# Optimization experiments

Hardware: AMD Instinct MI355X
Metric: run time of the kernel (lower is better)

The kernel has to match this reference:

```python
import jax, jax.numpy as jnp
import numpy as np

N0, N1, N2 = 100000, 25000, 6250
F = 128
OUT = 5


def _mean_agg(feat_src, src, dst, n_dst):
    # DGL copy_u + mean: segment mean over destination nodes (0 for isolated dst)
    s = jax.ops.segment_sum(feat_src[src], dst, num_segments=n_dst)
    cnt = jax.ops.segment_sum(jnp.ones_like(dst, dtype=feat_src.dtype), dst, num_segments=n_dst)
    return s / jnp.maximum(cnt, 1.0)[:, None]


def _graph_conv(feat, src, dst, W, b, n):
    # DGL GraphConv, norm='both': D_src^-1/2 gather-sum D_dst^-1/2, then linear
    dt = feat.dtype
    out_deg = jax.ops.segment_sum(jnp.ones_like(src, dtype=dt), src, num_segments=n)
    in_deg = jax.ops.segment_sum(jnp.ones_like(dst, dtype=dt), dst, num_segments=n)
    ns = jnp.where(out_deg > 0, out_deg ** -0.5, 0.0)
    nd = jnp.where(in_deg > 0, in_deg ** -0.5, 0.0)
    agg = jax.ops.segment_sum((feat * ns[:, None])[src], dst, num_segments=n)
    return (agg * nd[:, None]) @ W + b


def setup_inputs() -> dict:
    key = jax.random.key(0)
    keys = jax.random.split(key, 64)
    _c = iter(range(64))
    def nrm(shape, s=0.05):
        return jax.random.normal(keys[next(_c)], shape, dtype=jnp.float32) * s
    def ri(n, hi):
        return jax.random.randint(keys[next(_c)], (n,), 0, hi)
    inp = {
        'X': nrm((N0, 32), 1.0),
        'g0_src': ri(1600000, N0), 'g0_dst': ri(1600000, N0),
        'g1_src': ri(400000, N1), 'g1_dst': ri(400000, N1),
        'g2_src': ri(100000, N2), 'g2_dst': ri(100000, N2),
        'inc0_src': ri(100000, N0), 'inc0_dst': ri(100000, N1),
        'inc1_src': ri(25000, N1), 'inc1_dst': ri(25000, N2),
        'dec0_src': ri(100000, N2), 'dec0_dst': ri(100000, N1),
        'dec1_src': ri(400000, N1), 'dec1_dst': ri(400000, N0),
        'W_emb': nrm((32, F)), 'b_emb': jnp.zeros((F,), jnp.float32),
        'W_gcn0': nrm((F, F)), 'b_gcn0': jnp.zeros((F,), jnp.float32),
        'W_gcn1': nrm((F, F)), 'b_gcn1': jnp.zeros((F,), jnp.float32),
        'W_gcn2': nrm((F, F)), 'b_gcn2': jnp.zeros((F,), jnp.float32),
        'W_enc0': nrm((F, F)), 'b_enc0': jnp.zeros((F,), jnp.float32),
        'W_enc1': nrm((F, F)), 'b_enc1': jnp.zeros((F,), jnp.float32),
        'W_dec0': nrm((F, F)), 'b_dec0': jnp.zeros((F,), jnp.float32),
        'W_dec1': nrm((F, F)), 'b_dec1': jnp.zeros((F,), jnp.float32),
        'W_head0': nrm((2 * F, OUT)), 'b_head0': jnp.zeros((OUT,), jnp.float32),
        'W_head1': nrm((2 * F, OUT)), 'b_head1': jnp.zeros((OUT,), jnp.float32),
        'W_head2': nrm((2 * F, OUT)), 'b_head2': jnp.zeros((OUT,), jnp.float32),
    }
    return inp


def reference(X, g0_src, g0_dst, g1_src, g1_dst, g2_src, g2_dst,
              inc0_src, inc0_dst, inc1_src, inc1_dst,
              dec0_src, dec0_dst, dec1_src, dec1_dst,
              W_emb, b_emb, W_gcn0, b_gcn0, W_gcn1, b_gcn1, W_gcn2, b_gcn2,
              W_enc0, b_enc0, W_enc1, b_enc1, W_dec0, b_dec0, W_dec1, b_dec1,
              W_head0, b_head0, W_head1, b_head1, W_head2, b_head2):
    # embedding at finest scale
    h0 = X @ W_emb + b_emb                                   # [N0, F]
    # encode + pool fine -> coarse (copy_u/mean)
    h1 = _mean_agg(h0 @ W_enc0 + b_enc0, inc0_src, inc0_dst, N1)   # [N1, F]
    h2 = _mean_agg(h1 @ W_enc1 + b_enc1, inc1_src, inc1_dst, N2)   # [N2, F]
    # intra-scale GraphConv
    g0 = _graph_conv(h0, g0_src, g0_dst, W_gcn0, b_gcn0, N0)
    g1 = _graph_conv(h1, g1_src, g1_dst, W_gcn1, b_gcn1, N1)
    g2 = _graph_conv(h2, g2_src, g2_dst, W_gcn2, b_gcn2, N2)
    # decode coarse -> fine
    d2 = g2
    d1 = _mean_agg(d2 @ W_dec0 + b_dec0, dec0_src, dec0_dst, N1)   # [N1, F]
    d0 = _mean_agg(d1 @ W_dec1 + b_dec1, dec1_src, dec1_dst, N0)   # [N0, F]
    # per-scale heads with softmax
    o0 = jax.nn.softmax(jnp.concatenate([g0, d0], -1) @ W_head0 + b_head0, axis=-1)
    o1 = jax.nn.softmax(jnp.concatenate([g1, d1], -1) @ W_head1 + b_head1, axis=-1)
    o2 = jax.nn.softmax(jnp.concatenate([g2, d2], -1) @ W_head2 + b_head2, axis=-1)
    return jnp.concatenate([o0, o1, o2], axis=0)             # [N0+N1+N2, OUT]
```

## Files before the change

kernel.cpp:

```cpp
#include <hip/hip_runtime.h>

#define F 128
static const int N0 = 100000, N1 = 25000, N2 = 6250;

typedef unsigned short u16;
typedef unsigned int   u32;
typedef __attribute__((ext_vector_type(8))) short bf16x8;
typedef __attribute__((ext_vector_type(4))) float f32x4;

__device__ __forceinline__ float bf2f(u16 u) {
    union { u32 i; float f; } v; v.i = ((u32)u) << 16; return v.f;
}
__device__ __forceinline__ u16 f2bf(float f) {
    u32 u = __float_as_uint(f);
    u += 0x7fff + ((u >> 16) & 1);
    return (u16)(u >> 16);
}

struct Seg7 {
    const int* src[7];
    const int* dst[7];
    int end[7];
    int cbase[7];
    int obase[7];
};

#define EPT 4
#define CEPT 4
#define SM32  (64*(32+8)*2 + 128*(32+8)*2 + 128*4)
#define SM128 (64*(128+8)*2 + 128*(128+8)*2 + 128*4)


template <int K, bool AF32, bool MASK>
__device__ __forceinline__ void dev_mm(char* smem, const void* __restrict__ Ap,
                                       const float* __restrict__ W,
                                       const float* __restrict__ bias,
                                       u16* __restrict__ out,
                                       const int* __restrict__ rowptr,
                                       int M, int blk) {
    const int AST = K + 8;
    const int WST = K + 8;
    u16* Al = (u16*)smem;
    u16* Wt = (u16*)(smem + 64 * AST * 2);
    float* bl = (float*)(smem + 64 * AST * 2 + 128 * WST * 2);
    int tid = threadIdx.x;
    int m0 = blk * 64;

    for (int i = tid; i < K * 128; i += 256) {
        int k = i >> 7, n = i & 127;
        Wt[n * WST + k] = f2bf(W[i]);
    }
    for (int i = tid; i < 64 * K; i += 256) {
        int r = i / K, c = i % K;
        int gr = m0 + r;
        u16 v = 0;
        if (gr < M) {
            if (AF32) v = f2bf(((const float*)Ap)[(size_t)gr * K + c]);
            else      v = ((const u16*)Ap)[(size_t)gr * K + c];
        }
        Al[r * AST + c] = v;
    }
    if (tid < 128) bl[tid] = bias[tid];
    __syncthreads();

    int w = tid >> 6;
    int lane = tid & 63;
    int m16 = lane & 15;
    int quad = lane >> 4;

    f32x4 acc[8];
#pragma unroll
    for (int t = 0; t < 8; t++)
#pragma unroll
        for (int r = 0; r < 4; r++) acc[t][r] = 0.f;

    for (int k0 = 0; k0 < K; k0 += 32) {
        bf16x8 af = *(const bf16x8*)&Al[(w * 16 + m16) * AST + k0 + quad * 8];
#pragma unroll
        for (int t = 0; t < 8; t++) {
            bf16x8 bf = *(const bf16x8*)&Wt[(t * 16 + m16) * WST + k0 + quad * 8];
            acc[t] = __builtin_amdgcn_mfma_f32_16x16x32_bf16(af, bf, acc[t], 0, 0, 0);
        }
    }

#pragma unroll
    for (int t = 0; t < 8; t++) {
#pragma unroll
        for (int r = 0; r < 4; r++) {
            int gr = m0 + w * 16 + quad * 4 + r;
            if (gr >= M) continue;
            int gc = t * 16 + m16;
            bool zrow = false;
            if (MASK) zrow = (rowptr[gr + 1] == rowptr[gr]);
            float v = acc[t][r] + bl[gc];
            out[(size_t)gr * F + gc] = zrow ? (u16)0 : f2bf(v);
        }
    }
}

template <int MODE>
__device__ __forceinline__ void dev_gather(const u16* __restrict__ feat,
                                           const int* __restrict__ rowptr,
                                           const int* __restrict__ col,
                                           const float* __restrict__ odr,
                                           u16* __restrict__ out, int M, int blk) {
    int wv = (blk * 256 + (int)threadIdx.x) >> 6;
    if (wv >= M) return;
    int lane = threadIdx.x & 63;
    int fo = lane << 1;
    int beg = rowptr[wv], end = rowptr[wv + 1];
    float a0 = 0.f, a1 = 0.f;
    int j = beg;
    for (; j + 8 <= end; j += 8) {
        int cc[8];
#pragma unroll
        for (int t = 0; t < 8; t++) cc[t] = col[j + t];
        float ss[8];
#pragma unroll
        for (int t = 0; t < 8; t++) ss[t] = (MODE == 1) ? odr[cc[t]] : 1.f;
        ushort2 uu[8];
#pragma unroll
        for (int t = 0; t < 8; t++) uu[t] = *(const ushort2*)&feat[(size_t)cc[t] * F + fo];
#pragma unroll
        for (int t = 0; t < 8; t++) { a0 += bf2f(uu[t].x) * ss[t]; a1 += bf2f(uu[t].y) * ss[t]; }
    }
    for (; j < end; j++) {
        int c = col[j];
        float s = (MODE == 1) ? odr[c] : 1.f;
        ushort2 u = *(const ushort2*)&feat[(size_t)c * F + fo];
        a0 += bf2f(u.x) * s; a1 += bf2f(u.y) * s;
    }
    int deg = end - beg;
    float fs = (MODE == 0) ? (deg > 0 ? 1.f / (float)deg : 0.f)
                           : (deg > 0 ? rsqrtf((float)deg) : 0.f);
    ushort2 o; o.x = f2bf(a0 * fs); o.y = f2bf(a1 * fs);
    *(ushort2*)&out[(size_t)wv * F + fo] = o;
}

template <bool GD>
__device__ __forceinline__ void dev_head(char* smem, const u16* __restrict__ g,
                                         const u16* __restrict__ d,
                                         const int* __restrict__ rowptr,
                                         const int* __restrict__ col,
                                         const float* __restrict__ Wh,
                                         const float* __restrict__ bh,
                                         float* __restrict__ out, int M, int blk) {
    float* Wl = (float*)smem;
    float* bl = (float*)(smem + 1280 * 4);
    int tid = threadIdx.x;
    for (int i = tid; i < 1280; i += 256) Wl[i] = Wh[i];
    if (tid < 5) bl[tid] = bh[tid];
    __syncthreads();

    int lane = tid & 63;
    int wv = tid >> 6;
    int r0 = blk * 32 + wv * 8;
    int k0 = lane << 1;
    for (int i = 0; i < 8; i++) {
        int row = r0 + i;
        if (row < M) {
            float d0v, d1v;
            if (GD) {
                int beg = rowptr[row], end = rowptr[row + 1];
                d0v = 0.f; d1v = 0.f;
                int j = beg;
                for (; j + 4 <= end; j += 4) {
                    int c0 = col[j], c1 = col[j + 1], c2 = col[j + 2], c3 = col[j + 3];
                    ushort2 u0 = *(const ushort2*)&d[(size_t)c0 * F + k0];
                    ushort2 u1 = *(const ushort2*)&d[(size_t)c1 * F + k0];
                    ushort2 u2 = *(const ushort2*)&d[(size_t)c2 * F + k0];
                    ushort2 u3 = *(const ushort2*)&d[(size_t)c3 * F + k0];
                    d0v += bf2f(u0.x) + bf2f(u1.x) + bf2f(u2.x) + bf2f(u3.x);
                    d1v += bf2f(u0.y) + bf2f(u1.y) + bf2f(u2.y) + bf2f(u3.y);
                }
                for (; j < end; j++) {
                    int c = col[j];
                    ushort2 u = *(const ushort2*)&d[(size_t)c * F + k0];
                    d0v += bf2f(u.x); d1v += bf2f(u.y);
                }
                int deg = end - beg;
                float fs = deg > 0 ? 1.f / (float)deg : 0.f;
                d0v *= fs; d1v *= fs;
            } else {
                ushort2 du = *(const ushort2*)&d[(size_t)row * F + k0];
                d0v = bf2f(du.x); d1v = bf2f(du.y);
            }
            ushort2 gu = *(const ushort2*)&g[(size_t)row * F + k0];
            float g0v = bf2f(gu.x), g1v = bf2f(gu.y);
            float p[5];
#pragma unroll
            for (int o = 0; o < 5; o++) {
                p[o] = g0v * Wl[k0 * 5 + o] + g1v * Wl[(k0 + 1) * 5 + o] +
                       d0v * Wl[(k0 + 128) * 5 + o] + d1v * Wl[(k0 + 129) * 5 + o];
            }
#pragma unroll
            for (int o = 0; o < 5; o++) {
                float v = p[o];
                v += __shfl_xor(v, 32, 64);
                v += __shfl_xor(v, 16, 64);
                v += __shfl_xor(v, 8, 64);
                v += __shfl_xor(v, 4, 64);
                v += __shfl_xor(v, 2, 64);
                v += __shfl_xor(v, 1, 64);
                p[o] = v + bl[o];
            }
            if (lane == 0) {
                float m = p[0];
#pragma unroll
                for (int o = 1; o < 5; o++) m = fmaxf(m, p[o]);
                float e[5], s = 0.f;
#pragma unroll
                for (int o = 0; o < 5; o++) { e[o] = expf(p[o] - m); s += e[o]; }
                float inv = 1.f / s;
#pragma unroll
                for (int o = 0; o < 5; o++) out[(size_t)row * 5 + o] = e[o] * inv;
            }
        }
    }
}


__global__ __launch_bounds__(256) void k_count_emb(Seg7 S, int* __restrict__ cnt,
                                                   int* __restrict__ od,
                                                   u16* __restrict__ occ, int ETOT,
                                                   const float* __restrict__ X,
                                                   const float* __restrict__ Wemb,
                                                   const float* __restrict__ bemb,
                                                   u16* __restrict__ h0, int nbMM) {
    __shared__ char smem[SM32];
    if ((int)blockIdx.x < nbMM) {
        dev_mm<32, true, false>(smem, X, Wemb, bemb, h0, nullptr, N0, blockIdx.x);
        return;
    }
    int base = ((int)blockIdx.x - nbMM) * (256 * CEPT) + threadIdx.x;
    int ee[CEPT], grow[CEPT], gs[CEPT];
#pragma unroll
    for (int t = 0; t < CEPT; t++) {
        int e = base + t * 256;
        ee[t] = e;
        grow[t] = -1; gs[t] = -1;
        if (e < ETOT) {
            int s = 0;
            while (e >= S.end[s]) s++;
            int le = e - ((s == 0) ? 0 : S.end[s - 1]);
            grow[t] = S.cbase[s] + S.dst[s][le];
            int ob = S.obase[s];
            if (ob >= 0) gs[t] = ob + S.src[s][le];
        }
    }
    u32 r[CEPT];
#pragma unroll
    for (int t = 0; t < CEPT; t++)
        if (grow[t] >= 0) r[t] = atomicAdd((u32*)&cnt[grow[t]], 1u);
#pragma unroll
    for (int t = 0; t < CEPT; t++)
        if (grow[t] >= 0) occ[ee[t]] = (u16)r[t];
#pragma unroll
    for (int t = 0; t < CEPT; t++)
        if (gs[t] >= 0) atomicAdd(&od[gs[t]], 1);
}

__global__ __launch_bounds__(256) void k_fill_odr(Seg7 S,
                                                  const int* __restrict__ rowptr,
                                                  const u16* __restrict__ occ,
                                                  int* __restrict__ col, int ETOT,
                                                  float invRow, int nbFill,
                                                  const int* __restrict__ od,
                                                  float* __restrict__ odr, int nod) {
    if ((int)blockIdx.x >= nbFill) {
        int i = ((int)blockIdx.x - nbFill) * 256 + threadIdx.x;
        if (i < nod) { int o = od[i]; odr[i] = o > 0 ? rsqrtf((float)o) : 0.f; }
        return;
    }
    int win = blockIdx.x & 7;
    int base = ((int)blockIdx.x >> 3) * (256 * EPT) + threadIdx.x;
#pragma unroll
    for (int t = 0; t < EPT; t++) {
        int e = base + t * 256;
        if (e >= ETOT) break;
        int s = 0;
        while (e >= S.end[s]) s++;
        int le = e - ((s == 0) ? 0 : S.end[s - 1]);
        int grow = S.cbase[s] + S.dst[s][le];
        int w1 = (int)((float)grow * invRow); w1 = w1 > 7 ? 7 : w1;
        if (w1 == win) {
            col[rowptr[grow] + (int)occ[e]] = S.src[s][le];
        }
    }
}

#define SCHUNK 4096
__global__ __launch_bounds__(1024) void k_scan1(const int* __restrict__ cnt,
                                                int* __restrict__ partial, int n) {
    __shared__ int red[1024];
    int tid = threadIdx.x;
    int base = blockIdx.x * SCHUNK + tid * 4;
    int s = 0;
#pragma unroll
    for (int j = 0; j < 4; j++) { int i = base + j; if (i < n) s += cnt[i]; }
    red[tid] = s;
    __syncthreads();
    for (int d = 512; d > 0; d >>= 1) {
        if (tid < d) red[tid] += red[tid + d];
        __syncthreads();
    }
    if (tid == 0) partial[blockIdx.x] = red[0];
}

__global__ __launch_bounds__(128) void k_scan2(int* __restrict__ partial, int G) {
    __shared__ int sh[128];
    int tid = threadIdx.x;
    sh[tid] = (tid < G) ? partial[tid] : 0;
    __syncthreads();
    for (int d = 1; d < 128; d <<= 1) {
        int t = (tid >= d) ? sh[tid - d] : 0;
        __syncthreads();
        sh[tid] += t;
        __syncthreads();
    }
    if (tid < G) partial[tid] = (tid > 0) ? sh[tid - 1] : 0;
    if (tid == 127) partial[G] = sh[127];
}

__global__ __launch_bounds__(1024) void k_scan3(const int* __restrict__ cnt,
                                                const int* __restrict__ partial,
                                                int* __restrict__ rowptr,
                                                int n, int G) {
    __shared__ int red[1024];
    int tid = threadIdx.x;
    int base = blockIdx.x * SCHUNK + tid * 4;
    int v0 = 0, v1 = 0, v2 = 0, v3 = 0;
    if (base + 0 < n) v0 = cnt[base + 0];
    if (base + 1 < n) v1 = cnt[base + 1];
    if (base + 2 < n) v2 = cnt[base + 2];
    if (base + 3 < n) v3 = cnt[base + 3];
    red[tid] = v0 + v1 + v2 + v3;
    __syncthreads();
    for (int d = 1; d < 1024; d <<= 1) {
        int t = (tid >= d) ? red[tid - d] : 0;
        __syncthreads();
        red[tid] += t;
        __syncthreads();
    }
    int off = partial[blockIdx.x] + ((tid > 0) ? red[tid - 1] : 0);
    if (base + 0 < n) { rowptr[base + 0] = off; off += v0; }
    if (base + 1 < n) { rowptr[base + 1] = off; off += v1; }
    if (base + 2 < n) { rowptr[base + 2] = off; off += v2; }
    if (base + 3 < n) { rowptr[base + 3] = off; off += v3; }
    if (blockIdx.x == 0 && tid == 0) rowptr[n] = partial[G];
}

template <int MODE>
__global__ __launch_bounds__(256) void k_gather(const u16* __restrict__ feat,
                                                const int* __restrict__ rowptr,
                                                const int* __restrict__ col,
                                                const float* __restrict__ odr,
                                                u16* __restrict__ out, int M) {
    dev_gather<MODE>(feat, rowptr, col, odr, out, M, blockIdx.x);
}

template <int K, bool AF32, bool MASK>
__global__ __launch_bounds__(256) void k_mm(const void* __restrict__ Ap,
                                            const float* __restrict__ W,
                                            const float* __restrict__ bias,
                                            u16* __restrict__ out,
                                            const int* __restrict__ rowptr,
                                            int M) {
    __shared__ char smem[K == 32 ? SM32 : SM128];
    dev_mm<K, AF32, MASK>(smem, Ap, W, bias, out, rowptr, M, blockIdx.x);
}

template <int MA, int MB>
__global__ __launch_bounds__(256) void k_gather2(
    const u16* fA, const int* rpA, const float* oA, u16* outA, int MAr, int nbA,
    const u16* fB, const int* rpB, const float* oB, u16* outB, int MBr,
    const int* __restrict__ col) {
    if ((int)blockIdx.x < nbA) dev_gather<MA>(fA, rpA, col, oA, outA, MAr, blockIdx.x);
    else                       dev_gather<MB>(fB, rpB, col, oB, outB, MBr, blockIdx.x - nbA);
}

__global__ __launch_bounds__(256) void k_mm2(
    const u16* A1, const float* W1, const float* b1, u16* o1, const int* rp1, int M1, int nb1,
    const u16* A2, const float* W2, const float* b2, u16* o2, int M2) {
    __shared__ char smem[SM128];
    if ((int)blockIdx.x < nb1) dev_mm<128, false, true >(smem, A1, W1, b1, o1, rp1, M1, blockIdx.x);
    else                       dev_mm<128, false, false>(smem, A2, W2, b2, o2, nullptr, M2, blockIdx.x - nb1);
}

__global__ __launch_bounds__(256) void k_head3(
    const u16* Ga, const u16* dFeat, const int* rpD1, const int* colp,
    const float* Wa, const float* Ba, int nb0,
    const u16* Gb, const u16* Db, const float* Wb, const float* Bb, int nb1,
    const u16* Gc, const float* Wc, const float* Bc,
    float* __restrict__ out) {
    __shared__ char smem[1280 * 4 + 32];
    int b = blockIdx.x;
    if (b < nb0)            dev_head<true >(smem, Ga, dFeat, rpD1, colp, Wa, Ba, out, N0, b);
    else if (b < nb0 + nb1) dev_head<false>(smem, Gb, Db, nullptr, nullptr, Wb, Bb, out + (size_t)N0 * 5, N1, b - nb0);
    else                    dev_head<false>(smem, Gc, Gc, nullptr, nullptr, Wc, Bc, out + (size_t)(N0 + N1) * 5, N2, b - nb0 - nb1);
}

extern "C" void kernel_launch(void* const* d_in, const int* in_sizes, int n_in,
                              void* d_out, int out_size, void* d_ws, size_t ws_size,
                              hipStream_t stream) {
    const float* X = (const float*)d_in[0];
    const int *g0s = (const int*)d_in[1], *g0d = (const int*)d_in[2];
    const int *g1s = (const int*)d_in[3], *g1d = (const int*)d_in[4];
    const int *g2s = (const int*)d_in[5], *g2d = (const int*)d_in[6];
    const int *i0s = (const int*)d_in[7], *i0d = (const int*)d_in[8];
    const int *i1s = (const int*)d_in[9], *i1d = (const int*)d_in[10];
    const int *dc0s = (const int*)d_in[11], *dc0d = (const int*)d_in[12];
    const int *dc1s = (const int*)d_in[13], *dc1d = (const int*)d_in[14];
    const float *Wemb = (const float*)d_in[15], *bemb = (const float*)d_in[16];
    const float *Wg0 = (const float*)d_in[17], *bg0 = (const float*)d_in[18];
    const float *Wg1 = (const float*)d_in[19], *bg1 = (const float*)d_in[20];
    const float *Wg2 = (const float*)d_in[21], *bg2 = (const float*)d_in[22];
    const float *We0 = (const float*)d_in[23], *be0 = (const float*)d_in[24];
    const float *We1 = (const float*)d_in[25], *be1 = (const float*)d_in[26];
    const float *Wd0 = (const float*)d_in[27], *bd0 = (const float*)d_in[28];
    const float *Wd1 = (const float*)d_in[29], *bd1 = (const float*)d_in[30];
    const float *Wh0 = (const float*)d_in[31], *bh0 = (const float*)d_in[32];
    const float *Wh1 = (const float*)d_in[33], *bh1 = (const float*)d_in[34];
    const float *Wh2 = (const float*)d_in[35], *bh2 = (const float*)d_in[36];
    const int Eg0 = in_sizes[1], Eg1 = in_sizes[3], Eg2 = in_sizes[5];
    const int Ei0 = in_sizes[7], Ei1 = in_sizes[9];
    const int Ed0 = in_sizes[11], Ed1 = in_sizes[13];
    (void)n_in; (void)out_size; (void)ws_size;

    const int B_I0 = 0;
    const int B_I1 = B_I0 + N1;
    const int B_G2 = B_I1 + N2;
    const int B_D0 = B_G2 + N2;
    const int B_G1 = B_D0 + N1;
    const int B_G0 = B_G1 + N1;
    const int B_D1 = B_G0 + N0;
    const int NROWS = B_D1 + N0;
    const int ETOT  = Eg0 + Eg1 + Eg2 + Ei0 + Ei1 + Ed0 + Ed1;
    const int OB_G0 = 0, OB_G1 = N0, OB_G2 = N0 + N1;
    const int NOD = N0 + N1 + N2;
    const int G = (NROWS + SCHUNK - 1) / SCHUNK;
    const int rowsPerWin = (NROWS + 7) / 8;
    const float invRow = 1.0f / (float)rowsPerWin;
    const int NCH = (ETOT + 256 * EPT - 1) / (256 * EPT);

    char* wsb = (char*)d_ws;
    size_t off = 0;
    auto alloc = [&](size_t bytes) -> char* {
        char* p = wsb + off;
        off = (off + bytes + 255) & ~(size_t)255;
        return p;
    };
    u16* h0  = (u16*)alloc((size_t)N0 * F * 2);
    u16* h1  = (u16*)alloc((size_t)N1 * F * 2);
    u16* h2  = (u16*)alloc((size_t)N2 * F * 2);
    u16* G0  = (u16*)alloc((size_t)N0 * F * 2);
    u16* G1  = (u16*)alloc((size_t)N1 * F * 2);
    u16* G2  = (u16*)alloc((size_t)N2 * F * 2);
    u16* D1  = (u16*)alloc((size_t)N1 * F * 2);
    u16* agg = (u16*)alloc((size_t)N0 * F * 2);
    u16* bN1 = (u16*)alloc((size_t)N1 * F * 2);
    u16* bN2 = (u16*)alloc((size_t)N2 * F * 2);
    u16* pA  = D1;
    int* cnt    = (int*)alloc((size_t)NROWS * 4);
    int* od     = (int*)alloc((size_t)NOD * 4);
    int* rowptr = (int*)alloc((size_t)(NROWS + 1) * 4);
    u16* occ    = (u16*)alloc((size_t)ETOT * 2);
    float* odr  = (float*)alloc((size_t)NOD * 4);
    int* col    = (int*)alloc((size_t)ETOT * 4);
    int* part   = (int*)alloc((size_t)(G + 1) * 4);
    float* out = (float*)d_out;

    Seg7 S;
    S.src[0] = i0s;  S.dst[0] = i0d;  S.cbase[0] = B_I0; S.obase[0] = -1;
    S.src[1] = i1s;  S.dst[1] = i1d;  S.cbase[1] = B_I1; S.obase[1] = -1;
    S.src[2] = g2s;  S.dst[2] = g2d;  S.cbase[2] = B_G2; S.obase[2] = OB_G2;
    S.src[3] = dc0s; S.dst[3] = dc0d; S.cbase[3] = B_D0; S.obase[3] = -1;
    S.src[4] = g1s;  S.dst[4] = g1d;  S.cbase[4] = B_G1; S.obase[4] = OB_G1;
    S.src[5] = g0s;  S.dst[5] = g0d;  S.cbase[5] = B_G0; S.obase[5] = OB_G0;
    S.src[6] = dc1s; S.dst[6] = dc1d; S.cbase[6] = B_D1; S.obase[6] = -1;
    {
        int Es[7] = {Ei0, Ei1, Eg2, Ed0, Eg1, Eg0, Ed1};
        int acc = 0;
        for (int i = 0; i < 7; i++) { acc += Es[i]; S.end[i] = acc; }
    }

    const int nbEmb   = (N0 + 63) / 64;
    const int nbCount = (ETOT + 256 * CEPT - 1) / (256 * CEPT);
    const int nbFill  = NCH * 8;
    const int nbOdr   = (NOD + 255) / 256;

    hipMemsetAsync(cnt, 0, (size_t)((char*)od - (char*)cnt) + (size_t)NOD * 4, stream);
    k_count_emb<<<nbEmb + nbCount, 256, 0, stream>>>(S, cnt, od, occ, ETOT, X, Wemb, bemb, h0, nbEmb);
    k_scan1<<<G, 1024, 0, stream>>>(cnt, part, NROWS);
    k_scan2<<<1, 128, 0, stream>>>(part, G);
    k_scan3<<<G, 1024, 0, stream>>>(cnt, part, rowptr, NROWS, G);
    k_fill_odr<<<nbFill + nbOdr, 256, 0, stream>>>(S, rowptr, occ, col, ETOT, invRow, nbFill, od, odr, NOD);

    {
        int nbA = (N1 + 3) / 4, nbB = (N0 + 3) / 4;
        k_gather2<0, 1><<<nbA + nbB, 256, 0, stream>>>(
            h0, rowptr + B_I0, nullptr, pA, N1, nbA,
            h0, rowptr + B_G0, odr + OB_G0, agg, N0, col);
    }
    {
        int nb1 = (N1 + 63) / 64;
        int nb2 = (N0 + 63) / 64;
        k_mm2<<<nb1 + nb2, 256, 0, stream>>>(pA, We0, be0, h1, rowptr + B_I0, N1, nb1,
                                             agg, Wg0, bg0, G0, N0);
    }
    {
        int nbA = (N2 + 3) / 4, nbB = (N1 + 3) / 4;
        k_gather2<0, 1><<<nbA + nbB, 256, 0, stream>>>(
            h1, rowptr + B_I1, nullptr, bN2, N2, nbA,
            h1, rowptr + B_G1, odr + OB_G1, bN1, N1, col);
    }
    {
        int nb1 = (N2 + 63) / 64;
        int nb2 = (N1 + 63) / 64;
        k_mm2<<<nb1 + nb2, 256, 0, stream>>>(bN2, We1, be1, h2, rowptr + B_I1, N2, nb1,
                                             bN1, Wg1, bg1, G1, N1);
    }
    k_gather<1><<<(N2 + 3) / 4, 256, 0, stream>>>(h2, rowptr + B_G2, col, odr + OB_G2, bN2, N2);
    k_mm<128, false, false><<<(N2 + 63) / 64, 256, 0, stream>>>(bN2, Wg2, bg2, G2, nullptr, N2);
    k_mm<128, false, false><<<(N2 + 63) / 64, 256, 0, stream>>>(G2, Wd0, bd0, bN2, nullptr, N2);
    k_gather<0><<<(N1 + 3) / 4, 256, 0, stream>>>(bN2, rowptr + B_D0, col, nullptr, D1, N1);
    k_mm<128, false, false><<<(N1 + 63) / 64, 256, 0, stream>>>(D1, Wd1, bd1, bN1, nullptr, N1);
    {
        int nb0 = (N0 + 31) / 32, nb1 = (N1 + 31) / 32, nb2 = (N2 + 31) / 32;
        k_head3<<<nb0 + nb1 + nb2, 256, 0, stream>>>(G0, bN1, rowptr + B_D1, col, Wh0, bh0, nb0,
                                                     G1, D1, Wh1, bh1, nb1,
                                                     G2, Wh2, bh2, out);
    }
}
```

Baseline: 756.9 us.

## Move out-degree counting into windowed fill kernel and compute rsqrt inline in gather

Out-degree atomics move out of the count kernel and into the fill kernel. There they are split by node window across the eight block groups, so each group's atomics hit a localized range. The separate odr pass and buffer are gone: gathers read the integer out-degree and compute rsqrt on the fly. The count kernel also processes 8 edges per thread instead of 4. The trade-offs are that every window group now re-reads src for GCN segments, and gathers do extra rsqrt work for each edge.

Result: no change. 745.8 us (-1.5%).

```diff
diff --git a/kernel.cpp b/kernel.cpp
--- a/kernel.cpp
+++ b/kernel.cpp
@@ -26,7 +26,7 @@
 };
 
 #define EPT 4
-#define CEPT 4
+#define CEPT 8
 #define SM32  (64*(32+8)*2 + 128*(32+8)*2 + 128*4)
 #define SM128 (64*(128+8)*2 + 128*(128+8)*2 + 128*4)
 
@@ -102,7 +102,7 @@
 __device__ __forceinline__ void dev_gather(const u16* __restrict__ feat,
                                            const int* __restrict__ rowptr,
                                            const int* __restrict__ col,
-                                           const float* __restrict__ odr,
+                                           const int* __restrict__ od,
                                            u16* __restrict__ out, int M, int blk) {
     int wv = (blk * 256 + (int)threadIdx.x) >> 6;
     if (wv >= M) return;
@@ -117,7 +117,10 @@
         for (int t = 0; t < 8; t++) cc[t] = col[j + t];
         float ss[8];
 #pragma unroll
-        for (int t = 0; t < 8; t++) ss[t] = (MODE == 1) ? odr[cc[t]] : 1.f;
+        for (int t = 0; t < 8; t++) {
+            if (MODE == 1) { int o = od[cc[t]]; ss[t] = o > 0 ? rsqrtf((float)o) : 0.f; }
+            else ss[t] = 1.f;
+        }
         ushort2 uu[8];
 #pragma unroll
         for (int t = 0; t < 8; t++) uu[t] = *(const ushort2*)&feat[(size_t)cc[t] * F + fo];
@@ -126,7 +129,8 @@
     }
     for (; j < end; j++) {
         int c = col[j];
-        float s = (MODE == 1) ? odr[c] : 1.f;
+        float s = 1.f;
+        if (MODE == 1) { int o = od[c]; s = o > 0 ? rsqrtf((float)o) : 0.f; }
         ushort2 u = *(const ushort2*)&feat[(size_t)c * F + fo];
         a0 += bf2f(u.x) * s; a1 += bf2f(u.y) * s;
     }
@@ -221,7 +225,6 @@
 
 
 __global__ __launch_bounds__(256) void k_count_emb(Seg7 S, int* __restrict__ cnt,
-                                                   int* __restrict__ od,
                                                    u16* __restrict__ occ, int ETOT,
                                                    const float* __restrict__ X,
                                                    const float* __restrict__ Wemb,
@@ -233,19 +236,17 @@
         return;
     }
     int base = ((int)blockIdx.x - nbMM) * (256 * CEPT) + threadIdx.x;
-    int ee[CEPT], grow[CEPT], gs[CEPT];
+    int ee[CEPT], grow[CEPT];
 #pragma unroll
     for (int t = 0; t < CEPT; t++) {
         int e = base + t * 256;
         ee[t] = e;
-        grow[t] = -1; gs[t] = -1;
+        grow[t] = -1;
         if (e < ETOT) {
             int s = 0;
             while (e >= S.end[s]) s++;
             int le = e - ((s == 0) ? 0 : S.end[s - 1]);
             grow[t] = S.cbase[s] + S.dst[s][le];
-            int ob = S.obase[s];
-            if (ob >= 0) gs[t] = ob + S.src[s][le];
         }
     }
     u32 r[CEPT];
@@ -255,23 +256,14 @@
 #pragma unroll
     for (int t = 0; t < CEPT; t++)
         if (grow[t] >= 0) occ[ee[t]] = (u16)r[t];
-#pragma unroll
-    for (int t = 0; t < CEPT; t++)
-        if (gs[t] >= 0) atomicAdd(&od[gs[t]], 1);
-}
-
-__global__ __launch_bounds__(256) void k_fill_odr(Seg7 S,
-                                                  const int* __restrict__ rowptr,
-                                                  const u16* __restrict__ occ,
-                                                  int* __restrict__ col, int ETOT,
-                                                  float invRow, int nbFill,
-                                                  const int* __restrict__ od,
-                                                  float* __restrict__ odr, int nod) {
-    if ((int)blockIdx.x >= nbFill) {
-        int i = ((int)blockIdx.x - nbFill) * 256 + threadIdx.x;
-        if (i < nod) { int o = od[i]; odr[i] = o > 0 ? rsqrtf((float)o) : 0.f; }
-        return;
-    }
+}
+
+__global__ __launch_bounds__(256) void k_fill_od(Seg7 S,
+                                                 const int* __restrict__ rowptr,
+                                                 const u16* __restrict__ occ,
+                                                 int* __restrict__ col,
+                                                 int* __restrict__ od, int ETOT,
+                                                 float invRow, float invOd) {
     int win = blockIdx.x & 7;
     int base = ((int)blockIdx.x >> 3) * (256 * EPT) + threadIdx.x;
 #pragma unroll
@@ -283,8 +275,13 @@
         int le = e - ((s == 0) ? 0 : S.end[s - 1]);
         int grow = S.cbase[s] + S.dst[s][le];
         int w1 = (int)((float)grow * invRow); w1 = w1 > 7 ? 7 : w1;
-        if (w1 == win) {
-            col[rowptr[grow] + (int)occ[e]] = S.src[s][le];
+        int sv = -1;
+        if (w1 == win || S.obase[s] >= 0) sv = S.src[s][le];
+        if (w1 == win) col[rowptr[grow] + (int)occ[e]] = sv;
+        if (S.obase[s] >= 0) {
+            int gs = S.obase[s] + sv;
+            int w2 = (int)((float)gs * invOd); w2 = w2 > 7 ? 7 : w2;
+            if (w2 == win) atomicAdd(&od[gs], 1);
         }
     }
 }
@@ -354,9 +351,9 @@
 __global__ __launch_bounds__(256) void k_gather(const u16* __restrict__ feat,
                                                 const int* __restrict__ rowptr,
                                                 const int* __restrict__ col,
-                                                const float* __restrict__ odr,
+                                                const int* __restrict__ od,
                                                 u16* __restrict__ out, int M) {
-    dev_gather<MODE>(feat, rowptr, col, odr, out, M, blockIdx.x);
+    dev_gather<MODE>(feat, rowptr, col, od, out, M, blockIdx.x);
 }
 
 template <int K, bool AF32, bool MASK>
@@ -372,8 +369,8 @@
 
 template <int MA, int MB>
 __global__ __launch_bounds__(256) void k_gather2(
-    const u16* fA, const int* rpA, const float* oA, u16* outA, int MAr, int nbA,
-    const u16* fB, const int* rpB, const float* oB, u16* outB, int MBr,
+    const u16* fA, const int* rpA, const int* oA, u16* outA, int MAr, int nbA,
+    const u16* fB, const int* rpB, const int* oB, u16* outB, int MBr,
     const int* __restrict__ col) {
     if ((int)blockIdx.x < nbA) dev_gather<MA>(fA, rpA, col, oA, outA, MAr, blockIdx.x);
     else                       dev_gather<MB>(fB, rpB, col, oB, outB, MBr, blockIdx.x - nbA);
@@ -440,7 +437,9 @@
     const int NOD = N0 + N1 + N2;
     const int G = (NROWS + SCHUNK - 1) / SCHUNK;
     const int rowsPerWin = (NROWS + 7) / 8;
+    const int odPerWin   = (NOD + 7) / 8;
     const float invRow = 1.0f / (float)rowsPerWin;
+    const float invOd  = 1.0f / (float)odPerWin;
     const int NCH = (ETOT + 256 * EPT - 1) / (256 * EPT);
 
     char* wsb = (char*)d_ws;
@@ -465,7 +464,6 @@
     int* od     = (int*)alloc((size_t)NOD * 4);
     int* rowptr = (int*)alloc((size_t)(NROWS + 1) * 4);
     u16* occ    = (u16*)alloc((size_t)ETOT * 2);
-    float* odr  = (float*)alloc((size_t)NOD * 4);
     int* col    = (int*)alloc((size_t)ETOT * 4);
     int* part   = (int*)alloc((size_t)(G + 1) * 4);
     float* out = (float*)d_out;
@@ -487,20 +485,19 @@
     const int nbEmb   = (N0 + 63) / 64;
     const int nbCount = (ETOT + 256 * CEPT - 1) / (256 * CEPT);
     const int nbFill  = NCH * 8;
-    const int nbOdr   = (NOD + 255) / 256;
 
     hipMemsetAsync(cnt, 0, (size_t)((char*)od - (char*)cnt) + (size_t)NOD * 4, stream);
-    k_count_emb<<<nbEmb + nbCount, 256, 0, stream>>>(S, cnt, od, occ, ETOT, X, Wemb, bemb, h0, nbEmb);
+    k_count_emb<<<nbEmb + nbCount, 256, 0, stream>>>(S, cnt, occ, ETOT, X, Wemb, bemb, h0, nbEmb);
     k_scan1<<<G, 1024, 0, stream>>>(cnt, part, NROWS);
     k_scan2<<<1, 128, 0, stream>>>(part, G);
     k_scan3<<<G, 1024, 0, stream>>>(cnt, part, rowptr, NROWS, G);
-    k_fill_odr<<<nbFill + nbOdr, 256, 0, stream>>>(S, rowptr, occ, col, ETOT, invRow, nbFill, od, odr, NOD);
+    k_fill_od<<<nbFill, 256, 0, stream>>>(S, rowptr, occ, col, od, ETOT, invRow, invOd);
 
     {
         int nbA = (N1 + 3) / 4, nbB = (N0 + 3) / 4;
         k_gather2<0, 1><<<nbA + nbB, 256, 0, stream>>>(
             h0, rowptr + B_I0, nullptr, pA, N1, nbA,
-            h0, rowptr + B_G0, odr + OB_G0, agg, N0, col);
+            h0, rowptr + B_G0, od + OB_G0, agg, N0, col);
     }
     {
         int nb1 = (N1 + 63) / 64;
@@ -512,7 +509,7 @@
         int nbA = (N2 + 3) / 4, nbB = (N1 + 3) / 4;
         k_gather2<0, 1><<<nbA + nbB, 256, 0, stream>>>(
             h1, rowptr + B_I1, nullptr, bN2, N2, nbA,
-            h1, rowptr + B_G1, odr + OB_G1, bN1, N1, col);
+            h1, rowptr + B_G1, od + OB_G1, bN1, N1, col);
     }
     {
         int nb1 = (N2 + 63) / 64;
@@ -520,7 +517,7 @@
         k_mm2<<<nb1 + nb2, 256, 0, stream>>>(bN2, We1, be1, h2, rowptr + B_I1, N2, nb1,
                                              bN1, Wg1, bg1, G1, N1);
     }
-    k_gather<1><<<(N2 + 3) / 4, 256, 0, stream>>>(h2, rowptr + B_G2, col, odr + OB_G2, bN2, N2);
+    k_gather<1><<<(N2 + 3) / 4, 256, 0, stream>>>(h2, rowptr + B_G2, col, od + OB_G2, bN2, N2);
     k_mm<128, false, false><<<(N2 + 63) / 64, 256, 0, stream>>>(bN2, Wg2, bg2, G2, nullptr, N2);
     k_mm<128, false, false><<<(N2 + 63) / 64, 256, 0, stream>>>(G2, Wd0, bd0, bN2, nullptr, N2);
     k_gather<0><<<(N1 + 3) / 4, 256, 0, stream>>>(bN2, rowptr + B_D0, col, nullptr, D1, N1);
```
